# Optimization experiments

Hardware: AMD Instinct MI355X
Metric: run time of the kernel (lower is better)

The kernel has to match this reference:

```python
import jax, jax.numpy as jnp
import numpy as np

D_MODEL = 1024
N_HEADS = 16
HEAD_DIM = D_MODEL // N_HEADS
BASE = 10000.0


def _rope_cos_sin(seq_len):
    # inv_freq: [head_dim/2]
    inv_freq = 1.0 / (BASE ** (jnp.arange(0, HEAD_DIM, 2, dtype=jnp.float32) / HEAD_DIM))
    t = jnp.arange(seq_len, dtype=jnp.float32)
    freqs = jnp.outer(t, inv_freq)                 # [S, head_dim/2]
    emb = jnp.concatenate([freqs, freqs], axis=-1)  # [S, head_dim]
    return jnp.cos(emb), jnp.sin(emb)


def _rotate_half(x):
    x1, x2 = jnp.split(x, 2, axis=-1)
    return jnp.concatenate([-x2, x1], axis=-1)


def setup_inputs() -> dict:
    key = jax.random.key(0)
    ks = jax.random.split(key, 9)
    B, S, D = 2, 2048, D_MODEL
    sc = 1.0 / np.sqrt(D)
    return {
        "x": jax.random.normal(ks[0], (B, S, D), jnp.float32),
        "Wq": jax.random.normal(ks[1], (D, D), jnp.float32) * sc,
        "bq": jax.random.normal(ks[2], (D,), jnp.float32) * 0.01,
        "Wk": jax.random.normal(ks[3], (D, D), jnp.float32) * sc,
        "bk": jax.random.normal(ks[4], (D,), jnp.float32) * 0.01,
        "Wv": jax.random.normal(ks[5], (D, D), jnp.float32) * sc,
        "bv": jax.random.normal(ks[6], (D,), jnp.float32) * 0.01,
        "Wo": jax.random.normal(ks[7], (D, D), jnp.float32) * sc,
        "bo": jax.random.normal(ks[8], (D,), jnp.float32) * 0.01,
    }


def reference(x, Wq, bq, Wk, bk, Wv, bv, Wo, bo):
    B, S, D = x.shape
    H, Hd = N_HEADS, HEAD_DIM
    # projections (torch Linear: x @ W.T + b), reshape to [B, H, S, Hd]
    def proj(W, b):
        y = jnp.einsum('bsd,ed->bse', x, W) + b
        return y.reshape(B, S, H, Hd).transpose(0, 2, 1, 3)
    q, k, v = proj(Wq, bq), proj(Wk, bk), proj(Wv, bv)
    cos, sin = _rope_cos_sin(S)            # [S, Hd]
    cos = cos[None, None]                   # [1,1,S,Hd]
    sin = sin[None, None]
    q = q * cos + _rotate_half(q) * sin
    k = k * cos + _rotate_half(k) * sin
    scale = jnp.sqrt(jnp.float32(Hd))
    scores = jnp.einsum('bhqd,bhkd->bhqk', q, k) / scale  # [B,H,S,S]
    attn = jax.nn.softmax(scores, axis=-1)
    out = jnp.einsum('bhqk,bhkd->bhqd', attn, v)          # [B,H,S,Hd]
    out = out.transpose(0, 2, 1, 3).reshape(B, S, D)
    return jnp.einsum('bsd,ed->bse', out, Wo) + bo
```

## Files before the change

kernel.cpp:

```cpp
#include <hip/hip_runtime.h>
#include <hip/hip_fp16.h>
#include <math.h>

#define D_MODEL 1024
#define NH 16
#define HD 64
#define SEQ 2048
#define BATCH 2
#define MROWS (BATCH*SEQ)
#define KDIM 1024

typedef unsigned short u16;
typedef __attribute__((ext_vector_type(8))) _Float16 h8;
typedef __attribute__((ext_vector_type(8))) short s8v;
typedef __attribute__((ext_vector_type(4))) float f4v;

#define MFMAH(a, b, c) __builtin_amdgcn_mfma_f32_16x16x32_f16(a, b, c, 0, 0, 0)

__device__ __forceinline__ void gld16(const u16* g, u16* l) {
    __builtin_amdgcn_global_load_lds(
        (const __attribute__((address_space(1))) void*)g,
        (__attribute__((address_space(3))) void*)l, 16, 0, 0);
}

__device__ __forceinline__ u16 f32_to_f16(float f) {
    return __half_as_ushort(__float2half(f));
}

__global__ __launch_bounds__(256)
void convert_f16(const float* __restrict__ x,
                 const float* __restrict__ Wq, const float* __restrict__ Wk,
                 const float* __restrict__ Wv, const float* __restrict__ Wo,
                 u16* __restrict__ xF,
                 u16* __restrict__ WqF, u16* __restrict__ WkF,
                 u16* __restrict__ WvF, u16* __restrict__ WoF,
                 float2* __restrict__ ropeT) {
    int i = blockIdx.x * 256 + threadIdx.x;
    if (i >= (1 << 20)) {
        int idx2 = i - (1 << 20);
        int s  = idx2 >> 5;
        int dd = idx2 & 31;
        float inv = __expf(-(float)dd * 0.2878231366f);
        float ang = (float)s * inv;
        ropeT[idx2] = make_float2(cosf(ang), sinf(ang));
        return;
    }
    const float* src;
    u16* dst;
    int idx;
    if (i < (1 << 19)) {
        src = x; dst = xF; idx = i;
    } else {
        int j = i - (1 << 19);
        int w = j >> 17;
        idx = j & ((1 << 17) - 1);
        switch (w) {
            case 0:  src = Wq; dst = WqF; break;
            case 1:  src = Wk; dst = WkF; break;
            case 2:  src = Wv; dst = WvF; break;
            default: src = Wo; dst = WoF; break;
        }
    }
    float4 a = ((const float4*)src)[idx * 2];
    float4 b = ((const float4*)src)[idx * 2 + 1];
    s8v o;
    o[0] = (short)f32_to_f16(a.x); o[1] = (short)f32_to_f16(a.y);
    o[2] = (short)f32_to_f16(a.z); o[3] = (short)f32_to_f16(a.w);
    o[4] = (short)f32_to_f16(b.x); o[5] = (short)f32_to_f16(b.y);
    o[6] = (short)f32_to_f16(b.z); o[7] = (short)f32_to_f16(b.w);
    ((s8v*)dst)[idx] = o;
}

__global__ __launch_bounds__(256, 1)
void qkv_gemm(const u16* __restrict__ xF, const u16* __restrict__ WqF,
              const u16* __restrict__ WkF, const u16* __restrict__ WvF,
              const float* __restrict__ bq, const float* __restrict__ bk,
              const float* __restrict__ bv,
              const float2* __restrict__ ropeT,
              u16* __restrict__ QF, u16* __restrict__ KF,
              u16* __restrict__ VtF, float* __restrict__ km2) {
    __shared__ __align__(16) u16 SMEM[49152];

    const int t    = threadIdx.x;
    const int w    = t >> 6;
    const int lane = t & 63;
    const int quad = lane >> 4;
    const int l15  = lane & 15;
    const int wr   = w >> 1;
    const int wc   = w & 1;

    const int bid  = blockIdx.x;
    const int xcd  = bid & 7;
    const int j    = bid >> 3;
    const int m0   = (xcd * 2 + (j & 1)) * 256;
    const int yt   = j >> 1;
    const int wsel = yt >> 3;
    const int n0   = (yt & 7) * 128;

    const u16* Bg;
    const float* bias;
    if (wsel == 0)      { Bg = WqF; bias = bq; }
    else if (wsel == 1) { Bg = WkF; bias = bk; }
    else                { Bg = WvF; bias = bv; }

    const int lr = lane >> 3;
    const int lc = (((lane & 7) ^ lr)) * 8;

    f4v acc[8][4];
    #pragma unroll
    for (int i = 0; i < 8; i++)
        #pragma unroll
        for (int jj = 0; jj < 4; jj++)
            acc[i][jj] = (f4v){0.f, 0.f, 0.f, 0.f};

#define STAGE(K0, DB) do {                                                   \
    u16* As_ = SMEM + (DB);                                                  \
    u16* Bs_ = As_ + 16384;                                                  \
    _Pragma("unroll")                                                        \
    for (int jj_ = 0; jj_ < 8; jj_++) {                                      \
        int seg = jj_ * 4 + w;                                               \
        gld16(xF + (size_t)(m0 + seg * 8 + lr) * KDIM + (K0) + lc,           \
              As_ + seg * 512);                                              \
    }                                                                        \
    _Pragma("unroll")                                                        \
    for (int jj_ = 0; jj_ < 4; jj_++) {                                      \
        int seg = jj_ * 4 + w;                                               \
        gld16(Bg + (size_t)(n0 + seg * 8 + lr) * KDIM + (K0) + lc,           \
              Bs_ + seg * 512);                                              \
    }                                                                        \
} while (0)

    STAGE(0, 0);
    __syncthreads();

    int buf = 0;
    for (int k0 = 0; k0 < KDIM; k0 += 64) {
        if (k0 + 64 < KDIM) STAGE(k0 + 64, (buf ^ 1) * 24576);

        const u16* As = SMEM + buf * 24576;
        const u16* Bs = As + 16384;
        #pragma unroll
        for (int kk = 0; kk < 2; kk++) {
            const int swz = ((kk * 4 + quad) ^ (l15 & 7)) << 3;
            h8 a[8], b[4];
            #pragma unroll
            for (int mt = 0; mt < 8; mt++)
                a[mt] = *(const h8*)&As[(wr * 128 + mt * 16 + l15) * 64 + swz];
            #pragma unroll
            for (int nt = 0; nt < 4; nt++)
                b[nt] = *(const h8*)&Bs[(wc * 64 + nt * 16 + l15) * 64 + swz];
            #pragma unroll
            for (int mt = 0; mt < 8; mt++)
                #pragma unroll
                for (int nt = 0; nt < 4; nt++)
                    acc[mt][nt] = MFMAH(a[mt], b[nt], acc[mt][nt]);
        }
        __syncthreads();
        buf ^= 1;
    }
#undef STAGE

    const int bb = m0 >> 11;
    const int s0 = m0 & 2047;
    const int h0 = n0 >> 6;

    if (wsel < 2) {
        u16* OF = (wsel == 0) ? QF : KF;
        float kn_max = 0.f;
        #pragma unroll
        for (int mt = 0; mt < 8; mt++) {
            #pragma unroll
            for (int r = 0; r < 4; r++) {
                int R = wr * 128 + mt * 16 + quad * 4 + r;
                int s = s0 + R;
                float rowsum = 0.f;
                #pragma unroll
                for (int nt = 0; nt < 2; nt++) {
                    int col = wc * 64 + nt * 16 + l15;
                    int n1 = n0 + col;
                    int dd = n1 & 31;
                    float v1 = acc[mt][nt][r]     + bias[n1];
                    float v2 = acc[mt][nt + 2][r] + bias[n1 + 32];
                    float2 cssn = ropeT[(s << 5) | dd];
                    float cs  = cssn.x;
                    float sn  = cssn.y;
                    float r1 = v1 * cs - v2 * sn;
                    float r2 = v2 * cs + v1 * sn;
                    rowsum += v1 * v1 + v2 * v2;
                    SMEM[R * 128 + (((col >> 3) ^ (R & 15)) << 3) + (col & 7)]
                        = f32_to_f16(r1);
                    int col2 = col + 32;
                    SMEM[R * 128 + (((col2 >> 3) ^ (R & 15)) << 3) + (col2 & 7)]
                        = f32_to_f16(r2);
                }
                if (wsel == 1) {
                    rowsum += __shfl_xor(rowsum, 1, 64);
                    rowsum += __shfl_xor(rowsum, 2, 64);
                    rowsum += __shfl_xor(rowsum, 4, 64);
                    rowsum += __shfl_xor(rowsum, 8, 64);
                    kn_max = fmaxf(kn_max, rowsum);
                }
            }
        }
        if (wsel == 1) {
            kn_max = fmaxf(kn_max, __shfl_xor(kn_max, 16, 64));
            kn_max = fmaxf(kn_max, __shfl_xor(kn_max, 32, 64));
            if (lane == 0) atomicMax((int*)km2, __float_as_int(kn_max));
        }
        __syncthreads();
        #pragma unroll
        for (int cc = 0; cc < 16; cc++) {
            int idx  = cc * 256 + t;
            int hl   = idx >> 11;
            int rem  = idx & 2047;
            int R    = rem >> 3;
            int dch  = rem & 7;
            s8v val = *(const s8v*)&SMEM[R * 128 +
                          (((hl * 8 + dch) ^ (R & 15)) << 3)];
            *(s8v*)(OF + (((size_t)bb * NH + h0 + hl) * SEQ + s0 + R) * 64
                       + dch * 8) = val;
        }
    } else {
        #pragma unroll
        for (int mt = 0; mt < 8; mt++) {
            #pragma unroll
            for (int nt = 0; nt < 4; nt++) {
                int n = wc * 64 + nt * 16 + l15;
                float bv_ = bias[n0 + n];
                #pragma unroll
                for (int r = 0; r < 4; r++) {
                    int m = wr * 128 + mt * 16 + quad * 4 + r;
                    float v = acc[mt][nt][r] + bv_;
                    SMEM[n * 256 + (((m >> 3) ^ (n & 31)) << 3) + (m & 7)]
                        = f32_to_f16(v);
                }
            }
        }
        __syncthreads();
        #pragma unroll
        for (int cc = 0; cc < 16; cc++) {
            int idx = cc * 256 + t;
            int n   = idx >> 5;
            int mc  = idx & 31;
            int d   = n & 63;
            int hh  = n >> 6;
            size_t obase = ((size_t)((bb * NH + h0 + hh) * HD + d)) * SEQ + s0;
            s8v val = *(const s8v*)&SMEM[n * 256 + ((mc ^ (n & 31)) << 3)];
            *(s8v*)(VtF + obase + mc * 8) = val;
        }
    }
}

__global__ __launch_bounds__(256, 4)
void flash_attn(const u16* __restrict__ QF, const u16* __restrict__ KF,
                const u16* __restrict__ VtF,
                const float* __restrict__ kmax2,
                u16* __restrict__ AOF) {
    __shared__ __align__(16) u16 KS[2][32 * 72];
    __shared__ __align__(16) u16 VtS[2][64 * 40];
    __shared__ __align__(16) u16 PS[128 * 40];

    const int t    = threadIdx.x;
    const int w    = t >> 6;
    const int lane = t & 63;
    const int quad = lane >> 4;
    const int l15  = lane & 15;

    const int bid = blockIdx.x;
    const int xcd = bid & 7;
    const int j   = bid >> 3;
    const int bh  = xcd * 4 + (j & 3);
    const int q0  = (j >> 2) * 128;

    const size_t kvbase = (size_t)bh * SEQ * HD;
    const float km2 = kmax2[0];

    h8 qf[2][2];
    float m0[2][4];
    #pragma unroll
    for (int g = 0; g < 2; g++) {
        const u16* qp = QF + kvbase +
            (size_t)(q0 + g * 64 + w * 16 + l15) * HD + quad * 8;
        qf[g][0] = *(const h8*)qp;
        qf[g][1] = *(const h8*)(qp + 32);
        float qn2 = 0.f;
        #pragma unroll
        for (int st = 0; st < 2; st++)
            #pragma unroll
            for (int e = 0; e < 8; e++) {
                float v = (float)qf[g][st][e];
                qn2 += v * v;
            }
        qn2 += __shfl_xor(qn2, 16, 64);
        qn2 += __shfl_xor(qn2, 32, 64);
        #pragma unroll
        for (int r = 0; r < 4; r++) {
            int src = (lane & 48) | (quad * 4 + r);
            float qr = __shfl(qn2, src, 64);
            m0[g][r] = sqrtf(qr * km2) * 0.125f;
        }
    }

    f4v o[2][4];
    float lsum[2][4];
    #pragma unroll
    for (int g = 0; g < 2; g++)
        #pragma unroll
        for (int nt = 0; nt < 4; nt++) {
            o[g][nt] = (f4v){0.f, 0.f, 0.f, 0.f};
            lsum[g][nt] = 0.f;
        }

    for (int k0 = 0; k0 < SEQ; k0 += 64) {
        __syncthreads();

        {
            int row = t >> 3;
            int dc  = (t & 7) * 8;
            *(s8v*)&KS[0][row * 72 + dc] =
                *(const s8v*)(KF + kvbase + (size_t)(k0 + row) * HD + dc);
            *(s8v*)&KS[1][row * 72 + dc] =
                *(const s8v*)(KF + kvbase + (size_t)(k0 + 32 + row) * HD + dc);
        }
        {
            int d  = t >> 2;
            int kc = (t & 3) * 8;
            size_t g = (size_t)bh * HD * SEQ + (size_t)d * SEQ + k0 + kc;
            int col = kc ^ (((d >> 3) & 3) << 3);
            *(s8v*)&VtS[0][d * 40 + col] = *(const s8v*)(VtF + g);
            *(s8v*)&VtS[1][d * 40 + col] = *(const s8v*)(VtF + g + 32);
        }
        __syncthreads();

        #pragma unroll
        for (int sub = 0; sub < 2; sub++) {
            const u16* kb0 = KS[sub] + l15 * 72 + quad * 8;
            const u16* kb1 = KS[sub] + (16 + l15) * 72 + quad * 8;
            h8 kh0 = *(const h8*)kb0, kh1 = *(const h8*)(kb0 + 32);
            h8 kh2 = *(const h8*)kb1, kh3 = *(const h8*)(kb1 + 32);

            #pragma unroll
            for (int g = 0; g < 2; g++) {
                f4v s0 = (f4v){0.f, 0.f, 0.f, 0.f};
                f4v s1 = (f4v){0.f, 0.f, 0.f, 0.f};
                s0 = MFMAH(qf[g][0], kh0, s0);
                s0 = MFMAH(qf[g][1], kh1, s0);
                s1 = MFMAH(qf[g][0], kh2, s1);
                s1 = MFMAH(qf[g][1], kh3, s1);

                #pragma unroll
                for (int r = 0; r < 4; r++) {
                    float p0 = __expf(s0[r] * 0.125f - m0[g][r]);
                    float p1 = __expf(s1[r] * 0.125f - m0[g][r]);
                    lsum[g][r] += p0 + p1;
                    int row_l = g * 64 + w * 16 + quad * 4 + r;
                    int cs = row_l & 8;
                    PS[row_l * 40 + (l15 ^ cs)]        = f32_to_f16(p0);
                    PS[row_l * 40 + ((16 + l15) ^ cs)] = f32_to_f16(p1);
                }

                const int prow = g * 64 + w * 16 + l15;
                h8 ph = *(const h8*)&PS[prow * 40 + ((quad * 8) ^ (prow & 8))];
                #pragma unroll
                for (int nt = 0; nt < 4; nt++) {
                    int dim = nt * 16 + l15;
                    int voff = dim * 40 + ((quad * 8) ^ (((dim >> 3) & 3) << 3));
                    o[g][nt] = MFMAH(ph, *(const h8*)&VtS[sub][voff], o[g][nt]);
                }
            }
        }
    }

    const int b = bh >> 4;
    const int h = bh & 15;
    #pragma unroll
    for (int g = 0; g < 2; g++) {
        #pragma unroll
        for (int r = 0; r < 4; r++) {
            float l = lsum[g][r];
            l += __shfl_xor(l, 1, 64);
            l += __shfl_xor(l, 2, 64);
            l += __shfl_xor(l, 4, 64);
            l += __shfl_xor(l, 8, 64);
            float inv_l = 1.0f / l;
            int s = q0 + g * 64 + w * 16 + quad * 4 + r;
            size_t obase = (((size_t)b * SEQ + s) * NH + h) * HD;
            #pragma unroll
            for (int nt = 0; nt < 4; nt++) {
                AOF[obase + nt * 16 + l15] = f32_to_f16(o[g][nt][r] * inv_l);
            }
        }
    }
}

__global__ __launch_bounds__(256, 1)
void gemm_out(const u16* __restrict__ AF, const u16* __restrict__ BF,
              const float* __restrict__ bias, float* __restrict__ out) {
    __shared__ __align__(16) u16 SMEM[49152];

    const int t    = threadIdx.x;
    const int w    = t >> 6;
    const int lane = t & 63;
    const int quad = lane >> 4;
    const int l15  = lane & 15;
    const int wr   = w >> 1;
    const int wc   = w & 1;

    const int bid = blockIdx.x;
    const int xcd = bid & 7;
    const int j   = bid >> 3;
    const int m0  = (xcd * 2 + (j & 1)) * 256;
    const int n0  = (j >> 1) * 128;

    const int lr = lane >> 3;
    const int lc = (((lane & 7) ^ lr)) * 8;

    f4v acc[8][4];
    #pragma unroll
    for (int i = 0; i < 8; i++)
        #pragma unroll
        for (int jj = 0; jj < 4; jj++)
            acc[i][jj] = (f4v){0.f, 0.f, 0.f, 0.f};

#define STAGE(K0, DB) do {                                                   \
    u16* As_ = SMEM + (DB);                                                  \
    u16* Bs_ = As_ + 16384;                                                  \
    _Pragma("unroll")                                                        \
    for (int jj_ = 0; jj_ < 8; jj_++) {                                      \
        int seg = jj_ * 4 + w;                                               \
        gld16(AF + (size_t)(m0 + seg * 8 + lr) * KDIM + (K0) + lc,           \
              As_ + seg * 512);                                              \
    }                                                                        \
    _Pragma("unroll")                                                        \
    for (int jj_ = 0; jj_ < 4; jj_++) {                                      \
        int seg = jj_ * 4 + w;                                               \
        gld16(BF + (size_t)(n0 + seg * 8 + lr) * KDIM + (K0) + lc,           \
              Bs_ + seg * 512);                                              \
    }                                                                        \
} while (0)

    STAGE(0, 0);
    __syncthreads();

    int buf = 0;
    for (int k0 = 0; k0 < KDIM; k0 += 64) {
        if (k0 + 64 < KDIM) STAGE(k0 + 64, (buf ^ 1) * 24576);

        const u16* As = SMEM + buf * 24576;
        const u16* Bs = As + 16384;
        #pragma unroll
        for (int kk = 0; kk < 2; kk++) {
            const int swz = ((kk * 4 + quad) ^ (l15 & 7)) << 3;
            h8 a[8], b[4];
            #pragma unroll
            for (int mt = 0; mt < 8; mt++)
                a[mt] = *(const h8*)&As[(wr * 128 + mt * 16 + l15) * 64 + swz];
            #pragma unroll
            for (int nt = 0; nt < 4; nt++)
                b[nt] = *(const h8*)&Bs[(wc * 64 + nt * 16 + l15) * 64 + swz];
            #pragma unroll
            for (int mt = 0; mt < 8; mt++)
                #pragma unroll
                for (int nt = 0; nt < 4; nt++)
                    acc[mt][nt] = MFMAH(a[mt], b[nt], acc[mt][nt]);
        }
        __syncthreads();
        buf ^= 1;
    }
#undef STAGE

    #pragma unroll
    for (int mt = 0; mt < 8; mt++) {
        #pragma unroll
        for (int nt = 0; nt < 4; nt++) {
            int n = n0 + wc * 64 + nt * 16 + l15;
            float bv = bias[n];
            #pragma unroll
            for (int r = 0; r < 4; r++) {
                int m = m0 + wr * 128 + mt * 16 + quad * 4 + r;
                out[(size_t)m * 1024 + n] = acc[mt][nt][r] + bv;
            }
        }
    }
}

extern "C" void kernel_launch(void* const* d_in, const int* in_sizes, int n_in,
                              void* d_out, int out_size, void* d_ws, size_t ws_size,
                              hipStream_t stream) {
    const float* x  = (const float*)d_in[0];
    const float* Wq = (const float*)d_in[1];
    const float* bq = (const float*)d_in[2];
    const float* Wk = (const float*)d_in[3];
    const float* bk = (const float*)d_in[4];
    const float* Wv = (const float*)d_in[5];
    const float* bv = (const float*)d_in[6];
    const float* Wo = (const float*)d_in[7];
    const float* bo = (const float*)d_in[8];
    float* out = (float*)d_out;

    const size_t TEN = (size_t)MROWS * KDIM;
    const size_t WSZ = (size_t)KDIM * KDIM;

    u16* xF  = (u16*)d_ws;
    u16* WqF = xF + TEN;
    u16* WkF = WqF + WSZ;
    u16* WvF = WkF + WSZ;
    u16* WoF = WvF + WSZ;
    u16* QF  = WoF + WSZ;
    u16* KF  = QF + TEN;
    u16* VtF = KF + TEN;
    float* km2 = (float*)(VtF + TEN);
    float2* ropeT = (float2*)(km2 + 4);
    u16* AOF = xF;

    convert_f16<<<4352, 256, 0, stream>>>(x, Wq, Wk, Wv, Wo,
                                          xF, WqF, WkF, WvF, WoF, ropeT);

    hipMemsetAsync(km2, 0, 4, stream);

    qkv_gemm<<<384, 256, 0, stream>>>(xF, WqF, WkF, WvF,
                                      bq, bk, bv, ropeT, QF, KF, VtF, km2);

    flash_attn<<<512, 256, 0, stream>>>(QF, KF, VtF, km2, AOF);

    gemm_out<<<128, 256, 0, stream>>>(AOF, WoF, bo, out);
}
```

Baseline: 237.8 us.

## Shrink tiles in all three kernels to launch more blocks across CUs

The QKV GEMM and output GEMM now use 128-row tiles (the output GEMM also drops to 64 columns), with smaller LDS buffers and launch bounds that allow two blocks per CU. Flash attention handles 64 query rows per block instead of 128, doubling its grid. The aim is to fill the 256 CUs better, since the old grids of 128 to 512 blocks left many CUs idle or unbalanced. In exchange, each block reuses less data per tile, so more global and LDS traffic is spent per FLOP, and K/V tiles are reloaded by more attention blocks.

```diff
diff --git a/kernel.cpp b/kernel.cpp
--- a/kernel.cpp
+++ b/kernel.cpp
@@ -71,7 +71,7 @@
     ((s8v*)dst)[idx] = o;
 }
 
-__global__ __launch_bounds__(256, 1)
+__global__ __launch_bounds__(256, 2)
 void qkv_gemm(const u16* __restrict__ xF, const u16* __restrict__ WqF,
               const u16* __restrict__ WkF, const u16* __restrict__ WvF,
               const float* __restrict__ bq, const float* __restrict__ bk,
@@ -79,7 +79,7 @@
               const float2* __restrict__ ropeT,
               u16* __restrict__ QF, u16* __restrict__ KF,
               u16* __restrict__ VtF, float* __restrict__ km2) {
-    __shared__ __align__(16) u16 SMEM[49152];
+    __shared__ __align__(16) u16 SMEM[32768];
 
     const int t    = threadIdx.x;
     const int w    = t >> 6;
@@ -92,8 +92,8 @@
     const int bid  = blockIdx.x;
     const int xcd  = bid & 7;
     const int j    = bid >> 3;
-    const int m0   = (xcd * 2 + (j & 1)) * 256;
-    const int yt   = j >> 1;
+    const int m0   = (xcd * 4 + (j & 3)) * 128;
+    const int yt   = j >> 2;
     const int wsel = yt >> 3;
     const int n0   = (yt & 7) * 128;
 
@@ -106,25 +106,21 @@
     const int lr = lane >> 3;
     const int lc = (((lane & 7) ^ lr)) * 8;
 
-    f4v acc[8][4];
+    f4v acc[4][4];
     #pragma unroll
-    for (int i = 0; i < 8; i++)
+    for (int i = 0; i < 4; i++)
         #pragma unroll
         for (int jj = 0; jj < 4; jj++)
             acc[i][jj] = (f4v){0.f, 0.f, 0.f, 0.f};
 
 #define STAGE(K0, DB) do {                                                   \
     u16* As_ = SMEM + (DB);                                                  \
-    u16* Bs_ = As_ + 16384;                                                  \
+    u16* Bs_ = As_ + 8192;                                                   \
     _Pragma("unroll")                                                        \
-    for (int jj_ = 0; jj_ < 8; jj_++) {                                      \
+    for (int jj_ = 0; jj_ < 4; jj_++) {                                      \
         int seg = jj_ * 4 + w;                                               \
         gld16(xF + (size_t)(m0 + seg * 8 + lr) * KDIM + (K0) + lc,           \
               As_ + seg * 512);                                              \
-    }                                                                        \
-    _Pragma("unroll")                                                        \
-    for (int jj_ = 0; jj_ < 4; jj_++) {                                      \
-        int seg = jj_ * 4 + w;                                               \
         gld16(Bg + (size_t)(n0 + seg * 8 + lr) * KDIM + (K0) + lc,           \
               Bs_ + seg * 512);                                              \
     }                                                                        \
@@ -135,22 +131,22 @@
 
     int buf = 0;
     for (int k0 = 0; k0 < KDIM; k0 += 64) {
-        if (k0 + 64 < KDIM) STAGE(k0 + 64, (buf ^ 1) * 24576);
-
-        const u16* As = SMEM + buf * 24576;
-        const u16* Bs = As + 16384;
+        if (k0 + 64 < KDIM) STAGE(k0 + 64, (buf ^ 1) * 16384);
+
+        const u16* As = SMEM + buf * 16384;
+        const u16* Bs = As + 8192;
         #pragma unroll
         for (int kk = 0; kk < 2; kk++) {
             const int swz = ((kk * 4 + quad) ^ (l15 & 7)) << 3;
-            h8 a[8], b[4];
-            #pragma unroll
-            for (int mt = 0; mt < 8; mt++)
-                a[mt] = *(const h8*)&As[(wr * 128 + mt * 16 + l15) * 64 + swz];
+            h8 a[4], b[4];
+            #pragma unroll
+            for (int mt = 0; mt < 4; mt++)
+                a[mt] = *(const h8*)&As[(wr * 64 + mt * 16 + l15) * 64 + swz];
             #pragma unroll
             for (int nt = 0; nt < 4; nt++)
                 b[nt] = *(const h8*)&Bs[(wc * 64 + nt * 16 + l15) * 64 + swz];
             #pragma unroll
-            for (int mt = 0; mt < 8; mt++)
+            for (int mt = 0; mt < 4; mt++)
                 #pragma unroll
                 for (int nt = 0; nt < 4; nt++)
                     acc[mt][nt] = MFMAH(a[mt], b[nt], acc[mt][nt]);
@@ -168,10 +164,10 @@
         u16* OF = (wsel == 0) ? QF : KF;
         float kn_max = 0.f;
         #pragma unroll
-        for (int mt = 0; mt < 8; mt++) {
+        for (int mt = 0; mt < 4; mt++) {
             #pragma unroll
             for (int r = 0; r < 4; r++) {
-                int R = wr * 128 + mt * 16 + quad * 4 + r;
+                int R = wr * 64 + mt * 16 + quad * 4 + r;
                 int s = s0 + R;
                 float rowsum = 0.f;
                 #pragma unroll
@@ -209,10 +205,10 @@
         }
         __syncthreads();
         #pragma unroll
-        for (int cc = 0; cc < 16; cc++) {
+        for (int cc = 0; cc < 8; cc++) {
             int idx  = cc * 256 + t;
-            int hl   = idx >> 11;
-            int rem  = idx & 2047;
+            int hl   = idx >> 10;
+            int rem  = idx & 1023;
             int R    = rem >> 3;
             int dch  = rem & 7;
             s8v val = *(const s8v*)&SMEM[R * 128 +
@@ -222,30 +218,30 @@
         }
     } else {
         #pragma unroll
-        for (int mt = 0; mt < 8; mt++) {
+        for (int mt = 0; mt < 4; mt++) {
             #pragma unroll
             for (int nt = 0; nt < 4; nt++) {
                 int n = wc * 64 + nt * 16 + l15;
                 float bv_ = bias[n0 + n];
                 #pragma unroll
                 for (int r = 0; r < 4; r++) {
-                    int m = wr * 128 + mt * 16 + quad * 4 + r;
+                    int m = wr * 64 + mt * 16 + quad * 4 + r;
                     float v = acc[mt][nt][r] + bv_;
-                    SMEM[n * 256 + (((m >> 3) ^ (n & 31)) << 3) + (m & 7)]
+                    SMEM[n * 128 + (((m >> 3) ^ (n & 15)) << 3) + (m & 7)]
                         = f32_to_f16(v);
                 }
             }
         }
         __syncthreads();
         #pragma unroll
-        for (int cc = 0; cc < 16; cc++) {
+        for (int cc = 0; cc < 8; cc++) {
             int idx = cc * 256 + t;
-            int n   = idx >> 5;
-            int mc  = idx & 31;
+            int n   = idx >> 4;
+            int mc  = idx & 15;
             int d   = n & 63;
             int hh  = n >> 6;
             size_t obase = ((size_t)((bb * NH + h0 + hh) * HD + d)) * SEQ + s0;
-            s8v val = *(const s8v*)&SMEM[n * 256 + ((mc ^ (n & 31)) << 3)];
+            s8v val = *(const s8v*)&SMEM[n * 128 + ((mc ^ (n & 15)) << 3)];
             *(s8v*)(VtF + obase + mc * 8) = val;
         }
     }
@@ -258,7 +254,7 @@
                 u16* __restrict__ AOF) {
     __shared__ __align__(16) u16 KS[2][32 * 72];
     __shared__ __align__(16) u16 VtS[2][64 * 40];
-    __shared__ __align__(16) u16 PS[128 * 40];
+    __shared__ __align__(16) u16 PS[64 * 40];
 
     const int t    = threadIdx.x;
     const int w    = t >> 6;
@@ -270,25 +266,24 @@
     const int xcd = bid & 7;
     const int j   = bid >> 3;
     const int bh  = xcd * 4 + (j & 3);
-    const int q0  = (j >> 2) * 128;
+    const int q0  = (j >> 2) * 64;
 
     const size_t kvbase = (size_t)bh * SEQ * HD;
     const float km2 = kmax2[0];
 
-    h8 qf[2][2];
-    float m0[2][4];
-    #pragma unroll
-    for (int g = 0; g < 2; g++) {
+    h8 qf[2];
+    float mb[4];
+    {
         const u16* qp = QF + kvbase +
-            (size_t)(q0 + g * 64 + w * 16 + l15) * HD + quad * 8;
-        qf[g][0] = *(const h8*)qp;
-        qf[g][1] = *(const h8*)(qp + 32);
+            (size_t)(q0 + w * 16 + l15) * HD + quad * 8;
+        qf[0] = *(const h8*)qp;
+        qf[1] = *(const h8*)(qp + 32);
         float qn2 = 0.f;
         #pragma unroll
         for (int st = 0; st < 2; st++)
             #pragma unroll
             for (int e = 0; e < 8; e++) {
-                float v = (float)qf[g][st][e];
+                float v = (float)qf[st][e];
                 qn2 += v * v;
             }
         qn2 += __shfl_xor(qn2, 16, 64);
@@ -297,19 +292,17 @@
         for (int r = 0; r < 4; r++) {
             int src = (lane & 48) | (quad * 4 + r);
             float qr = __shfl(qn2, src, 64);
-            m0[g][r] = sqrtf(qr * km2) * 0.125f;
-        }
-    }
-
-    f4v o[2][4];
-    float lsum[2][4];
+            mb[r] = sqrtf(qr * km2) * 0.125f;
+        }
+    }
+
+    f4v o[4];
+    float lsum[4];
     #pragma unroll
-    for (int g = 0; g < 2; g++)
-        #pragma unroll
-        for (int nt = 0; nt < 4; nt++) {
-            o[g][nt] = (f4v){0.f, 0.f, 0.f, 0.f};
-            lsum[g][nt] = 0.f;
-        }
+    for (int nt = 0; nt < 4; nt++) {
+        o[nt] = (f4v){0.f, 0.f, 0.f, 0.f};
+        lsum[nt] = 0.f;
+    }
 
     for (int k0 = 0; k0 < SEQ; k0 += 64) {
         __syncthreads();
@@ -339,34 +332,31 @@
             h8 kh0 = *(const h8*)kb0, kh1 = *(const h8*)(kb0 + 32);
             h8 kh2 = *(const h8*)kb1, kh3 = *(const h8*)(kb1 + 32);
 
-            #pragma unroll
-            for (int g = 0; g < 2; g++) {
-                f4v s0 = (f4v){0.f, 0.f, 0.f, 0.f};
-                f4v s1 = (f4v){0.f, 0.f, 0.f, 0.f};
-                s0 = MFMAH(qf[g][0], kh0, s0);
-                s0 = MFMAH(qf[g][1], kh1, s0);
-                s1 = MFMAH(qf[g][0], kh2, s1);
-                s1 = MFMAH(qf[g][1], kh3, s1);
-
-                #pragma unroll
-                for (int r = 0; r < 4; r++) {
-                    float p0 = __expf(s0[r] * 0.125f - m0[g][r]);
-                    float p1 = __expf(s1[r] * 0.125f - m0[g][r]);
-                    lsum[g][r] += p0 + p1;
-                    int row_l = g * 64 + w * 16 + quad * 4 + r;
-                    int cs = row_l & 8;
-                    PS[row_l * 40 + (l15 ^ cs)]        = f32_to_f16(p0);
-                    PS[row_l * 40 + ((16 + l15) ^ cs)] = f32_to_f16(p1);
-                }
-
-                const int prow = g * 64 + w * 16 + l15;
-                h8 ph = *(const h8*)&PS[prow * 40 + ((quad * 8) ^ (prow & 8))];
-                #pragma unroll
-                for (int nt = 0; nt < 4; nt++) {
-                    int dim = nt * 16 + l15;
-                    int voff = dim * 40 + ((quad * 8) ^ (((dim >> 3) & 3) << 3));
-                    o[g][nt] = MFMAH(ph, *(const h8*)&VtS[sub][voff], o[g][nt]);
-                }
+            f4v sc0 = (f4v){0.f, 0.f, 0.f, 0.f};
+            f4v sc1 = (f4v){0.f, 0.f, 0.f, 0.f};
+            sc0 = MFMAH(qf[0], kh0, sc0);
+            sc0 = MFMAH(qf[1], kh1, sc0);
+            sc1 = MFMAH(qf[0], kh2, sc1);
+            sc1 = MFMAH(qf[1], kh3, sc1);
+
+            #pragma unroll
+            for (int r = 0; r < 4; r++) {
+                float p0 = __expf(sc0[r] * 0.125f - mb[r]);
+                float p1 = __expf(sc1[r] * 0.125f - mb[r]);
+                lsum[r] += p0 + p1;
+                int row_l = w * 16 + quad * 4 + r;
+                int cs = row_l & 8;
+                PS[row_l * 40 + (l15 ^ cs)]        = f32_to_f16(p0);
+                PS[row_l * 40 + ((16 + l15) ^ cs)] = f32_to_f16(p1);
+            }
+
+            const int prow = w * 16 + l15;
+            h8 ph = *(const h8*)&PS[prow * 40 + ((quad * 8) ^ (prow & 8))];
+            #pragma unroll
+            for (int nt = 0; nt < 4; nt++) {
+                int dim = nt * 16 + l15;
+                int voff = dim * 40 + ((quad * 8) ^ (((dim >> 3) & 3) << 3));
+                o[nt] = MFMAH(ph, *(const h8*)&VtS[sub][voff], o[nt]);
             }
         }
     }
@@ -374,29 +364,26 @@
     const int b = bh >> 4;
     const int h = bh & 15;
     #pragma unroll
-    for (int g = 0; g < 2; g++) {
-        #pragma unroll
-        for (int r = 0; r < 4; r++) {
-            float l = lsum[g][r];
-            l += __shfl_xor(l, 1, 64);
-            l += __shfl_xor(l, 2, 64);
-            l += __shfl_xor(l, 4, 64);
-            l += __shfl_xor(l, 8, 64);
-            float inv_l = 1.0f / l;
-            int s = q0 + g * 64 + w * 16 + quad * 4 + r;
-            size_t obase = (((size_t)b * SEQ + s) * NH + h) * HD;
-            #pragma unroll
-            for (int nt = 0; nt < 4; nt++) {
-                AOF[obase + nt * 16 + l15] = f32_to_f16(o[g][nt][r] * inv_l);
-            }
-        }
-    }
-}
-
-__global__ __launch_bounds__(256, 1)
+    for (int r = 0; r < 4; r++) {
+        float l = lsum[r];
+        l += __shfl_xor(l, 1, 64);
+        l += __shfl_xor(l, 2, 64);
+        l += __shfl_xor(l, 4, 64);
+        l += __shfl_xor(l, 8, 64);
+        float inv_l = 1.0f / l;
+        int s = q0 + w * 16 + quad * 4 + r;
+        size_t obase = (((size_t)b * SEQ + s) * NH + h) * HD;
+        #pragma unroll
+        for (int nt = 0; nt < 4; nt++) {
+            AOF[obase + nt * 16 + l15] = f32_to_f16(o[nt][r] * inv_l);
+        }
+    }
+}
+
+__global__ __launch_bounds__(256, 2)
 void gemm_out(const u16* __restrict__ AF, const u16* __restrict__ BF,
               const float* __restrict__ bias, float* __restrict__ out) {
-    __shared__ __align__(16) u16 SMEM[49152];
+    __shared__ __align__(16) u16 SMEM[24576];
 
     const int t    = threadIdx.x;
     const int w    = t >> 6;
@@ -409,30 +396,30 @@
     const int bid = blockIdx.x;
     const int xcd = bid & 7;
     const int j   = bid >> 3;
-    const int m0  = (xcd * 2 + (j & 1)) * 256;
-    const int n0  = (j >> 1) * 128;
+    const int m0  = (xcd * 4 + (j & 3)) * 128;
+    const int n0  = (j >> 2) * 64;
 
     const int lr = lane >> 3;
     const int lc = (((lane & 7) ^ lr)) * 8;
 
-    f4v acc[8][4];
+    f4v acc[4][2];
     #pragma unroll
-    for (int i = 0; i < 8; i++)
-        #pragma unroll
-        for (int jj = 0; jj < 4; jj++)
+    for (int i = 0; i < 4; i++)
+        #pragma unroll
+        for (int jj = 0; jj < 2; jj++)
             acc[i][jj] = (f4v){0.f, 0.f, 0.f, 0.f};
 
 #define STAGE(K0, DB) do {                                                   \
     u16* As_ = SMEM + (DB);                                                  \
-    u16* Bs_ = As_ + 16384;                                                  \
+    u16* Bs_ = As_ + 8192;                                                   \
     _Pragma("unroll")                                                        \
-    for (int jj_ = 0; jj_ < 8; jj_++) {                                      \
+    for (int jj_ = 0; jj_ < 4; jj_++) {                                      \
         int seg = jj_ * 4 + w;                                               \
         gld16(AF + (size_t)(m0 + seg * 8 + lr) * KDIM + (K0) + lc,           \
               As_ + seg * 512);                                              \
     }                                                                        \
     _Pragma("unroll")                                                        \
-    for (int jj_ = 0; jj_ < 4; jj_++) {                                      \
+    for (int jj_ = 0; jj_ < 2; jj_++) {                                      \
         int seg = jj_ * 4 + w;                                               \
         gld16(BF + (size_t)(n0 + seg * 8 + lr) * KDIM + (K0) + lc,           \
               Bs_ + seg * 512);                                              \
@@ -444,24 +431,24 @@
 
     int buf = 0;
     for (int k0 = 0; k0 < KDIM; k0 += 64) {
-        if (k0 + 64 < KDIM) STAGE(k0 + 64, (buf ^ 1) * 24576);
-
-        const u16* As = SMEM + buf * 24576;
-        const u16* Bs = As + 16384;
+        if (k0 + 64 < KDIM) STAGE(k0 + 64, (buf ^ 1) * 12288);
+
+        const u16* As = SMEM + buf * 12288;
+        const u16* Bs = As + 8192;
         #pragma unroll
         for (int kk = 0; kk < 2; kk++) {
             const int swz = ((kk * 4 + quad) ^ (l15 & 7)) << 3;
-            h8 a[8], b[4];
-            #pragma unroll
-            for (int mt = 0; mt < 8; mt++)
-                a[mt] = *(const h8*)&As[(wr * 128 + mt * 16 + l15) * 64 + swz];
-            #pragma unroll
-            for (int nt = 0; nt < 4; nt++)
-                b[nt] = *(const h8*)&Bs[(wc * 64 + nt * 16 + l15) * 64 + swz];
-            #pragma unroll
-            for (int mt = 0; mt < 8; mt++)
+            h8 a[4], b[2];
+            #pragma unroll
+            for (int mt = 0; mt < 4; mt++)
+                a[mt] = *(const h8*)&As[(wr * 64 + mt * 16 + l15) * 64 + swz];
+            #pragma unroll
+            for (int nt = 0; nt < 2; nt++)
+                b[nt] = *(const h8*)&Bs[(wc * 32 + nt * 16 + l15) * 64 + swz];
+            #pragma unroll
+            for (int mt = 0; mt < 4; mt++)
                 #pragma unroll
-                for (int nt = 0; nt < 4; nt++)
+                for (int nt = 0; nt < 2; nt++)
                     acc[mt][nt] = MFMAH(a[mt], b[nt], acc[mt][nt]);
         }
         __syncthreads();
@@ -470,14 +457,14 @@
 #undef STAGE
 
     #pragma unroll
-    for (int mt = 0; mt < 8; mt++) {
-        #pragma unroll
-        for (int nt = 0; nt < 4; nt++) {
-            int n = n0 + wc * 64 + nt * 16 + l15;
+    for (int mt = 0; mt < 4; mt++) {
+        #pragma unroll
+        for (int nt = 0; nt < 2; nt++) {
+            int n = n0 + wc * 32 + nt * 16 + l15;
             float bv = bias[n];
             #pragma unroll
             for (int r = 0; r < 4; r++) {
-                int m = m0 + wr * 128 + mt * 16 + quad * 4 + r;
+                int m = m0 + wr * 64 + mt * 16 + quad * 4 + r;
                 out[(size_t)m * 1024 + n] = acc[mt][nt][r] + bv;
             }
         }
@@ -518,10 +505,10 @@
 
     hipMemsetAsync(km2, 0, 4, stream);
 
-    qkv_gemm<<<384, 256, 0, stream>>>(xF, WqF, WkF, WvF,
+    qkv_gemm<<<768, 256, 0, stream>>>(xF, WqF, WkF, WvF,
                                       bq, bk, bv, ropeT, QF, KF, VtF, km2);
 
-    flash_attn<<<512, 256, 0, stream>>>(QF, KF, VtF, km2, AOF);
-
-    gemm_out<<<128, 256, 0, stream>>>(AOF, WoF, bo, out);
-}
+    flash_attn<<<1024, 256, 0, stream>>>(QF, KF, VtF, km2, AOF);
+
+    gemm_out<<<512, 256, 0, stream>>>(AOF, WoF, bo, out);
+}
```

After: 210.6 us. 1.13x faster.
